# Performance work log

Measured on AMD Instinct MI355X. Metric: run time of the kernel, lower is better.

Reference implementation:

```python
import jax, jax.numpy as jnp
import numpy as np

NQ = 4
PI_HALF = np.pi / 2
HAD = jnp.array([[1, 1], [1, -1]], dtype=jnp.complex64) / np.sqrt(2)
CNOT = jnp.array([[1, 0, 0, 0], [0, 1, 0, 0], [0, 0, 0, 1], [0, 0, 1, 0]], dtype=jnp.complex64)
_bits = (np.arange(2 ** NQ)[:, None] >> np.arange(NQ - 1, -1, -1)[None, :]) & 1
ZSIGNS = jnp.asarray(1.0 - 2.0 * _bits, jnp.float32)  # [16, NQ]


def _ry(theta):
    c = jnp.cos(theta / 2).astype(jnp.complex64)
    s = jnp.sin(theta / 2).astype(jnp.complex64)
    return jnp.stack([jnp.stack([c, -s], -1), jnp.stack([s, c], -1)], -2)  # [...,2,2]


def _rot(phi, theta, omega):
    # PennyLane Rot = RZ(omega) @ RY(theta) @ RZ(phi)
    c = jnp.cos(theta / 2).astype(jnp.complex64)
    s = jnp.sin(theta / 2).astype(jnp.complex64)
    ep = jnp.exp(0.5j * phi).astype(jnp.complex64)
    eo = jnp.exp(0.5j * omega).astype(jnp.complex64)
    return jnp.stack([jnp.stack([jnp.conj(ep) * jnp.conj(eo) * c, -ep * jnp.conj(eo) * s]),
                      jnp.stack([jnp.conj(ep) * eo * s, ep * eo * c])])


def _cry(theta):
    # controlled-RY, batched: [B] -> [B,4,4], basis order (control, target)
    B = theta.shape[0]
    U = jnp.zeros((B, 4, 4), jnp.complex64).at[:, 0, 0].set(1.0).at[:, 1, 1].set(1.0)
    return U.at[:, 2:, 2:].set(_ry(theta))


def _apply1(state, U, wire):
    s = jnp.moveaxis(state, wire + 1, 1)
    shp = s.shape
    s = s.reshape(shp[0], 2, -1)
    s = jnp.einsum('ij,bjk->bik', U, s) if U.ndim == 2 else jnp.einsum('bij,bjk->bik', U, s)
    return jnp.moveaxis(s.reshape(shp), 1, wire + 1)


def _apply2(state, U, q0, q1):
    s = jnp.moveaxis(state, (q0 + 1, q1 + 1), (1, 2))
    shp = s.shape
    s = s.reshape(shp[0], 4, -1)
    s = jnp.einsum('ij,bjk->bik', U, s) if U.ndim == 2 else jnp.einsum('bij,bjk->bik', U, s)
    return jnp.moveaxis(s.reshape(shp), (1, 2), (q0 + 1, q1 + 1))


def _init_state(B):
    s = jnp.zeros((B, 2 ** NQ), jnp.complex64).at[:, 0].set(1.0)
    return s.reshape((B,) + (2,) * NQ)


def _zexp(state):
    p = state.reshape(state.shape[0], -1)
    p = p.real ** 2 + p.imag ** 2
    return p @ ZSIGNS  # [B, NQ]


def _attention_circuit(q, k, params):
    # q, k: [E, NQ] angles; params: [NQ, 3] shared
    s = _init_state(q.shape[0])
    for i in range(NQ):
        s = _apply1(s, _ry(q[:, i]), i)
    for i in range(NQ):
        s = _apply1(s, HAD, i)
    for i in range(NQ):
        s = _apply2(s, _cry(k[:, i]), i, (i + 1) % NQ)
    for i in range(NQ):
        s = _apply1(s, _rot(params[i, 0], params[i, 1], params[i, 2]), i)
    return _zexp(s)


def _entangle_circuit(x, params):
    # x: [N, NQ] angles; params: [n_layers, NQ, 3]
    s = _init_state(x.shape[0])
    for i in range(NQ):
        s = _apply1(s, _ry(x[:, i]), i)
    for l in range(params.shape[0]):
        for i in range(NQ - 1):
            s = _apply2(s, CNOT, i, i + 1)
        for i in range(NQ):
            s = _apply1(s, _rot(params[l, i, 0], params[l, i, 1], params[l, i, 2]), i)
        s = _apply2(s, CNOT, 0, NQ - 1)  # n_qubits >= 4
    return _zexp(s)


def _path_circuit(x, params):
    # x: [N, NQ]; params: [3, NQ, 3]
    s = _init_state(x.shape[0])
    for i in range(NQ):
        s = _apply1(s, HAD, i)
    for i in range(NQ):
        s = _apply1(s, _ry(x[:, i]), i)
    for l in range(3):
        for i in range(NQ):
            s = _apply1(s, _rot(params[l, i, 0], params[l, i, 1], params[l, i, 2]), i)
        for i in range(NQ - 1):
            s = _apply2(s, CNOT, i, i + 1)
    return _zexp(s)


def _forward(x, W_in, b_in, lin_W, lin_b, qproj_W, qproj_b, ent_params,
             attq_W, attq_b, attk_W, attk_b, att_qp, path_params,
             path_in_W, path_in_b, path_out_W, path_out_b, out_W, out_b, edge_index):
    N = x.shape[0]
    loops = jnp.arange(N, dtype=edge_index.dtype)
    ei = jnp.concatenate([edge_index, jnp.stack([loops, loops])], axis=1)  # add_self_loops
    src, dst = ei[0], ei[1]
    h = jax.nn.relu(x @ W_in.T + b_in)
    for l in range(lin_W.shape[0]):
        x_cls = h @ lin_W[l].T + lin_b[l]
        xq = _entangle_circuit(jnp.tanh(h[:, :NQ]) * PI_HALF, ent_params[l])
        x_comb = x_cls + xq @ qproj_W[l].T + qproj_b[l]
        q = jnp.tanh(h @ attq_W[l].T + attq_b[l]) * PI_HALF
        k = jnp.tanh(h @ attk_W[l].T + attk_b[l]) * PI_HALF
        scores = _attention_circuit(q[src], k[dst], att_qp[l]).mean(axis=1)  # [E]
        att = jax.nn.softmax(scores)  # global softmax over all edges (faithful)
        h = jax.ops.segment_sum(att[:, None] * x_comb[src], dst, num_segments=N)
        h = jax.nn.relu(h)  # dropout is identity at eval
    pq = jnp.tanh(h @ path_in_W.T + path_in_b) * PI_HALF
    h = _path_circuit(pq, path_params) @ path_out_W.T + path_out_b
    return h @ out_W.T + out_b


def setup_inputs() -> dict:
    key = jax.random.key(0)
    ks = jax.random.split(key, 22)
    N, E, D_in, D_h, D_out, L = 20000, 300000, 64, 128, 32, 2
    w = lambda k, shape: jax.random.normal(k, shape, jnp.float32) * 0.1
    return {
        'x': jax.random.normal(ks[0], (N, D_in), jnp.float32),
        'W_in': w(ks[1], (D_h, D_in)), 'b_in': w(ks[2], (D_h,)),
        'lin_W': w(ks[3], (L, D_h, D_h)), 'lin_b': w(ks[4], (L, D_h)),
        'qproj_W': w(ks[5], (L, D_h, NQ)), 'qproj_b': w(ks[6], (L, D_h)),
        'ent_params': w(ks[7], (L, 2, NQ, 3)),
        'attq_W': w(ks[8], (L, NQ, D_h)), 'attq_b': w(ks[9], (L, NQ)),
        'attk_W': w(ks[10], (L, NQ, D_h)), 'attk_b': w(ks[11], (L, NQ)),
        'att_qp': w(ks[12], (L, NQ, 3)),
        'path_params': w(ks[13], (3, NQ, 3)),
        'path_in_W': w(ks[14], (NQ, D_h)), 'path_in_b': w(ks[15], (NQ,)),
        'path_out_W': w(ks[16], (D_h, NQ)), 'path_out_b': w(ks[17], (D_h,)),
        'out_W': w(ks[18], (D_out, D_h)), 'out_b': w(ks[19], (D_out,)),
        'edge_index': jax.random.randint(ks[20], (2, E), 0, N, dtype=jnp.int32),
    }


def reference(x, W_in, b_in, lin_W, lin_b, qproj_W, qproj_b, ent_params,
              attq_W, attq_b, attk_W, attk_b, att_qp, path_params,
              path_in_W, path_in_b, path_out_W, path_out_b, out_W, out_b, edge_index):
    return _forward(x, W_in, b_in, lin_W, lin_b, qproj_W, qproj_b, ent_params,
                    attq_W, attq_b, attk_W, attk_b, att_qp, path_params,
                    path_in_W, path_in_b, path_out_W, path_out_b, out_W, out_b, edge_index)
```

## Files before the change

kernel.cpp:

```cpp
#include <hip/hip_runtime.h>
#include <math.h>

#define PI_HALF 1.57079632679489662f

__device__ __forceinline__ float fast_tanh(float x) {
    float e = __expf(2.f * x);
    return 1.f - 2.f * __builtin_amdgcn_rcpf(e + 1.f);
}


__device__ __forceinline__ void prod_init(float sr[16],
        float c0, float s0, float c1, float s1,
        float c2, float s2, float c3, float s3) {
    float p2[4];
    p2[0] = c0 * c1; p2[1] = c0 * s1; p2[2] = s0 * c1; p2[3] = s0 * s1;
    float p3[8];
#pragma unroll
    for (int j = 0; j < 4; ++j) { p3[2 * j] = p2[j] * c2; p3[2 * j + 1] = p2[j] * s2; }
#pragma unroll
    for (int j = 0; j < 8; ++j) { sr[2 * j] = p3[j] * c3; sr[2 * j + 1] = p3[j] * s3; }
}

template<int M>
__device__ __forceinline__ void had_r(float sr[16]) {
    const float r = 0.70710678118654752f;
#pragma unroll
    for (int i = 0; i < 16; ++i) {
        if (i & M) continue;
        const int j = i | M;
        float ar = sr[i], br = sr[j];
        sr[i] = (ar + br) * r;
        sr[j] = (ar - br) * r;
    }
}

template<int MC, int MT>
__device__ __forceinline__ void cry_r(float sr[16], float c, float s) {
#pragma unroll
    for (int i = 0; i < 16; ++i) {
        if (!(i & MC) || (i & MT)) continue;
        const int j = i | MT;
        float ar = sr[i], br = sr[j];
        sr[i] = c * ar - s * br;
        sr[j] = s * ar + c * br;
    }
}

template<int MC, int MT>
__device__ __forceinline__ void cnot_r(float sr[16]) {
#pragma unroll
    for (int i = 0; i < 16; ++i) {
        if (!(i & MC) || (i & MT)) continue;
        const int j = i | MT;
        float t = sr[i]; sr[i] = sr[j]; sr[j] = t;
    }
}

template<int MC, int MT>
__device__ __forceinline__ void cnot_g(float sr[16], float si[16]) {
#pragma unroll
    for (int i = 0; i < 16; ++i) {
        if (!(i & MC) || (i & MT)) continue;
        const int j = i | MT;
        float tr = sr[i], ti = si[i];
        sr[i] = sr[j]; si[i] = si[j];
        sr[j] = tr;    si[j] = ti;
    }
}

template<int M>
__device__ __forceinline__ void rot_pre(float sr[16], float si[16], const float* __restrict__ u) {
    const float u00r = u[0], u00i = u[1], u01r = u[2], u01i = u[3];
    const float u10r = u[4], u10i = u[5], u11r = u[6], u11i = u[7];
#pragma unroll
    for (int i = 0; i < 16; ++i) {
        if (i & M) continue;
        const int j = i | M;
        float ar = sr[i], ai = si[i], br = sr[j], bi = si[j];
        sr[i] = u00r * ar - u00i * ai + u01r * br - u01i * bi;
        si[i] = u00r * ai + u00i * ar + u01r * bi + u01i * br;
        sr[j] = u10r * ar - u10i * ai + u11r * br - u11i * bi;
        si[j] = u10r * ai + u10i * ar + u11r * bi + u11i * br;
    }
}

template<int M>
__device__ __forceinline__ void rot_first(float sr[16], float si[16], const float* __restrict__ u) {
    const float u00r = u[0], u00i = u[1], u01r = u[2], u01i = u[3];
    const float u10r = u[4], u10i = u[5], u11r = u[6], u11i = u[7];
#pragma unroll
    for (int i = 0; i < 16; ++i) {
        if (i & M) continue;
        const int j = i | M;
        float ar = sr[i], br = sr[j];
        sr[i] = u00r * ar + u01r * br;
        si[i] = u00i * ar + u01i * br;
        sr[j] = u10r * ar + u11r * br;
        si[j] = u10i * ar + u11i * br;
    }
}

__device__ __forceinline__ void zexp_g(const float sr[16], const float si[16], float z[4]) {
    float p[16];
#pragma unroll
    for (int i = 0; i < 16; ++i) p[i] = sr[i] * sr[i] + si[i] * si[i];
    z[0] = z[1] = z[2] = z[3] = 0.f;
#pragma unroll
    for (int i = 0; i < 16; ++i) {
        z[0] += (i & 8) ? -p[i] : p[i];
        z[1] += (i & 4) ? -p[i] : p[i];
        z[2] += (i & 2) ? -p[i] : p[i];
        z[3] += (i & 1) ? -p[i] : p[i];
    }
}


__global__ void k_fsi(const int* __restrict__ ei, int* __restrict__ cur,
                      int* __restrict__ srcs, int* __restrict__ inv, int E, int EP,
                      const float* __restrict__ entp, const float* __restrict__ attqp,
                      const float* __restrict__ pparm,
                      const float* __restrict__ outW, const float* __restrict__ outb,
                      const float* __restrict__ poW, const float* __restrict__ pob,
                      float* __restrict__ rotbuf, float* __restrict__ M,
                      float* __restrict__ v,
                      const float* __restrict__ x, const float* __restrict__ W,
                      const float* __restrict__ b, float* __restrict__ h,
                      int N, int eblocks) {
    __shared__ float xs[32 * 64];
    const int bb = blockIdx.x;
    const int tid = threadIdx.x;
    if (bb < eblocks) {
        int e = bb * 256 + tid;
        if (e < EP) {
            int s_, d_;
            if (e < E) { s_ = ei[e]; d_ = ei[E + e]; } else { s_ = d_ = e - E; }
            int pos = atomicAdd(&cur[d_], 1);
            srcs[pos] = s_;
            inv[e] = pos;
        }
        return;
    }
    if (bb == eblocks) {
        const int t = tid;
        if (t < 36) {
            const float* p;
            if (t < 16)      p = entp  + t * 3;
            else if (t < 24) p = attqp + (t - 16) * 3;
            else             p = pparm + (t - 24) * 3;
            float phi = p[0], theta = p[1], omega = p[2];
            float st, ct; sincosf(0.5f * theta, &st, &ct);
            float sp, cp; sincosf(0.5f * (phi + omega), &sp, &cp);
            float sm, cm; sincosf(0.5f * (phi - omega), &sm, &cm);
            float* u = rotbuf + t * 8;
            u[0] =  ct * cp;  u[1] = -ct * sp;
            u[2] = -st * cm;  u[3] = -st * sm;
            u[4] =  st * cm;  u[5] = -st * sm;
            u[6] =  ct * cp;  u[7] =  ct * sp;
        } else if (t >= 64 && t < 192) {
            int t2 = t - 64;
            int o = t2 >> 2, i = t2 & 3;
            float acc = 0.f;
            for (int j = 0; j < 128; ++j) acc += outW[o * 128 + j] * poW[j * 4 + i];
            M[t2] = acc;
        } else if (t >= 192 && t < 224) {
            int o = t - 192;
            float acc = outb[o];
            for (int j = 0; j < 128; ++j) acc += outW[o * 128 + j] * pob[j];
            v[o] = acc;
        }
        return;
    }
    const int base = (bb - eblocks - 1) * 32;
    for (int idx = tid; idx < 32 * 64; idx += 256) {
        int n = base + (idx >> 6);
        xs[idx] = (n < N) ? x[(size_t)n * 64 + (idx & 63)] : 0.f;
    }
    __syncthreads();
    const int ch = tid & 127;
    const int half = tid >> 7;
    float acc[16];
#pragma unroll
    for (int n = 0; n < 16; ++n) acc[n] = 0.f;
    const float4* wr4 = (const float4*)(W + ch * 64);
    for (int c4 = 0; c4 < 16; ++c4) {
        float4 w = wr4[c4];
#pragma unroll
        for (int n = 0; n < 16; ++n) {
            float4 hv = *(const float4*)&xs[(half * 16 + n) * 64 + c4 * 4];
            acc[n] += w.x * hv.x + w.y * hv.y + w.z * hv.z + w.w * hv.w;
        }
    }
    const float bbv = b[ch];
#pragma unroll
    for (int n = 0; n < 16; ++n) {
        int node = base + half * 16 + n;
        if (node < N) h[(size_t)node * 128 + ch] = fmaxf(acc[n] + bbv, 0.f);
    }
}

__global__ void k_entlin(const float* __restrict__ h, const float* __restrict__ rotE2,
                         const float* __restrict__ linW, const float* __restrict__ linb,
                         const float* __restrict__ qpW, const float* __restrict__ qpb,
                         const float* __restrict__ aqW, const float* __restrict__ aqb,
                         const float* __restrict__ akW, const float* __restrict__ akb,
                         float* __restrict__ xcomb, float* __restrict__ qbuf,
                         float* __restrict__ kbuf, int N) {
    __shared__ float hs[16 * 128];
    __shared__ float xqs[16 * 4];
    const int base = blockIdx.x * 16;
    const int tid = threadIdx.x;
    for (int idx = tid; idx < 16 * 128; idx += 128) {
        int n = base + (idx >> 7);
        hs[idx] = (n < N) ? h[(size_t)n * 128 + (idx & 127)] : 0.f;
    }
    __syncthreads();
    if (tid < 16) {
        float4 hv = *(const float4*)&hs[tid * 128];
        float c0, s0, c1, s1, c2, s2, c3, s3;
        { float a = fast_tanh(hv.x) * (0.5f * PI_HALF); __sincosf(a, &s0, &c0); }
        { float a = fast_tanh(hv.y) * (0.5f * PI_HALF); __sincosf(a, &s1, &c1); }
        { float a = fast_tanh(hv.z) * (0.5f * PI_HALF); __sincosf(a, &s2, &c2); }
        { float a = fast_tanh(hv.w) * (0.5f * PI_HALF); __sincosf(a, &s3, &c3); }
        float sr[16], si[16];
        prod_init(sr, c0, s0, c1, s1, c2, s2, c3, s3);
        cnot_r<8, 4>(sr); cnot_r<4, 2>(sr); cnot_r<2, 1>(sr);
        rot_first<8>(sr, si, rotE2);
        rot_pre<4>(sr, si, rotE2 + 8);
        rot_pre<2>(sr, si, rotE2 + 16);
        rot_pre<1>(sr, si, rotE2 + 24);
        cnot_g<8, 1>(sr, si);
        cnot_g<8, 4>(sr, si); cnot_g<4, 2>(sr, si); cnot_g<2, 1>(sr, si);
        const float* P = rotE2 + 32;
        rot_pre<8>(sr, si, P);
        rot_pre<4>(sr, si, P + 8);
        rot_pre<2>(sr, si, P + 16);
        rot_pre<1>(sr, si, P + 24);
        cnot_g<8, 1>(sr, si);
        float z[4]; zexp_g(sr, si, z);
        xqs[tid * 4 + 0] = z[0]; xqs[tid * 4 + 1] = z[1];
        xqs[tid * 4 + 2] = z[2]; xqs[tid * 4 + 3] = z[3];
    }
    __syncthreads();
    float acc[16];
#pragma unroll
    for (int n = 0; n < 16; ++n) acc[n] = 0.f;
    const float4* wr4 = (const float4*)(linW + tid * 128);
    for (int c4 = 0; c4 < 32; ++c4) {
        float4 w = wr4[c4];
#pragma unroll
        for (int n = 0; n < 16; ++n) {
            float4 hv = *(const float4*)&hs[n * 128 + c4 * 4];
            acc[n] += w.x * hv.x + w.y * hv.y + w.z * hv.z + w.w * hv.w;
        }
    }
    const float bb = linb[tid] + qpb[tid];
    const float qw0 = qpW[tid * 4 + 0], qw1 = qpW[tid * 4 + 1];
    const float qw2 = qpW[tid * 4 + 2], qw3 = qpW[tid * 4 + 3];
#pragma unroll
    for (int n = 0; n < 16; ++n) {
        int node = base + n;
        if (node < N) {
            xcomb[(size_t)node * 128 + tid] = acc[n] + bb
                + qw0 * xqs[n * 4 + 0] + qw1 * xqs[n * 4 + 1]
                + qw2 * xqs[n * 4 + 2] + qw3 * xqs[n * 4 + 3];
        }
    }
    const int nl = tid >> 3;
    const int which = tid & 7;
    const int qi = which & 3;
    const float4* Wp4 = (const float4*)(((which < 4) ? aqW : akW) + qi * 128);
    float dot = (which < 4) ? aqb[qi] : akb[qi];
    for (int c4 = 0; c4 < 32; ++c4) {
        float4 w = Wp4[c4];
        float4 hv = *(const float4*)&hs[nl * 128 + c4 * 4];
        dot += w.x * hv.x + w.y * hv.y + w.z * hv.z + w.w * hv.w;
    }
    int node = base + nl;
    if (node < N) {
        float halfang = fast_tanh(dot) * (0.5f * PI_HALF);
        float s, c; __sincosf(halfang, &s, &c);
        float* dst = ((which < 4) ? qbuf : kbuf) + (size_t)node * 8 + qi * 2;
        dst[0] = c; dst[1] = s;
    }
}

__global__ void k_att(const float* __restrict__ qb, const float* __restrict__ kb,
                      const int* __restrict__ ei, const float* __restrict__ RA,
                      const int* __restrict__ inv, float* __restrict__ escore,
                      float* __restrict__ sumexp, int E, int EP) {
    __shared__ float red[4];
    int e = blockIdx.x * blockDim.x + threadIdx.x;
    float ex = 0.f;
    if (e < EP) {
        int s_, d_;
        if (e < E) { s_ = ei[e]; d_ = ei[E + e]; } else { s_ = d_ = e - E; }
        float4 qa = *(const float4*)&qb[(size_t)s_ * 8];
        float4 qc = *(const float4*)&qb[(size_t)s_ * 8 + 4];
        float4 ka = *(const float4*)&kb[(size_t)d_ * 8];
        float4 kc = *(const float4*)&kb[(size_t)d_ * 8 + 4];
        float sr[16], si[16];
        prod_init(sr, qa.x, qa.y, qa.z, qa.w, qc.x, qc.y, qc.z, qc.w);
        had_r<8>(sr); had_r<4>(sr); had_r<2>(sr); had_r<1>(sr);
        cry_r<8, 4>(sr, ka.x, ka.y);
        cry_r<4, 2>(sr, ka.z, ka.w);
        cry_r<2, 1>(sr, kc.x, kc.y);
        cry_r<1, 8>(sr, kc.z, kc.w);
        rot_first<8>(sr, si, RA);
        rot_pre<4>(sr, si, RA + 8);
        rot_pre<2>(sr, si, RA + 16);
        rot_pre<1>(sr, si, RA + 24);
        float p0  = sr[0]  * sr[0]  + si[0]  * si[0];
        float p1  = sr[1]  * sr[1]  + si[1]  * si[1];
        float p2  = sr[2]  * sr[2]  + si[2]  * si[2];
        float p4  = sr[4]  * sr[4]  + si[4]  * si[4];
        float p8  = sr[8]  * sr[8]  + si[8]  * si[8];
        float p7  = sr[7]  * sr[7]  + si[7]  * si[7];
        float p11 = sr[11] * sr[11] + si[11] * si[11];
        float p13 = sr[13] * sr[13] + si[13] * si[13];
        float p14 = sr[14] * sr[14] + si[14] * si[14];
        float p15 = sr[15] * sr[15] + si[15] * si[15];
        float sc = (p0 - p15) + 0.5f * ((p1 + p2 + p4 + p8) - (p7 + p11 + p13 + p14));
        ex = __expf(sc);
        escore[inv[e]] = ex;
    }
    float wsum = ex;
#pragma unroll
    for (int d = 32; d; d >>= 1) wsum += __shfl_xor(wsum, d, 64);
    if ((threadIdx.x & 63) == 0) red[threadIdx.x >> 6] = wsum;
    __syncthreads();
    if (threadIdx.x == 0) atomicAdd(sumexp, red[0] + red[1] + red[2] + red[3]);
}


__global__ void k_hist(const int* __restrict__ ei, int* __restrict__ cnt, int E, int EP) {
    int e = blockIdx.x * blockDim.x + threadIdx.x;
    if (e >= EP) return;
    int d_ = (e < E) ? ei[E + e] : e - E;
    atomicAdd(&cnt[d_], 1);
}

__global__ void k_scan(const int* __restrict__ cnt, int* __restrict__ off,
                       int* __restrict__ cur, int N) {
    __shared__ int tot[1024];
    const int t = threadIdx.x;
    const int chunk = (N + 1023) >> 10;
    const int s0 = t * chunk;
    const int s1 = min(s0 + chunk, N);
    int sum = 0;
    for (int i = s0; i < s1; ++i) sum += cnt[i];
    tot[t] = sum;
    __syncthreads();
    for (int d = 1; d < 1024; d <<= 1) {
        int v = (t >= d) ? tot[t - d] : 0;
        __syncthreads();
        tot[t] += v;
        __syncthreads();
    }
    int run = (t == 0) ? 0 : tot[t - 1];
    for (int i = s0; i < s1; ++i) {
        off[i] = run; cur[i] = run;
        run += cnt[i];
    }
}

__global__ void k_gather(const float* __restrict__ xcomb, const int* __restrict__ srcs,
                         const float* __restrict__ escore, const int* __restrict__ off,
                         const int* __restrict__ cnt, const float* __restrict__ sumexp,
                         float* __restrict__ h) {
    __shared__ int sS[128];
    __shared__ float wS[128];
    const int b = blockIdx.x;
    const int tid = threadIdx.x;
    const int start = off[b];
    const int num = cnt[b];
    float acc = 0.f;
    for (int base = 0; base < num; base += 128) {
        int m = min(128, num - base);
        if (tid < m) {
            sS[tid] = srcs[start + base + tid];
            wS[tid] = escore[start + base + tid];
        }
        __syncthreads();
        for (int i = 0; i < m; ++i)
            acc += wS[i] * xcomb[(size_t)sS[i] * 128 + tid];
        __syncthreads();
    }
    const float invS = __builtin_amdgcn_rcpf(sumexp[0]);
    h[(size_t)b * 128 + tid] = fmaxf(acc * invS, 0.f);
}

__global__ void k_tail(const float* __restrict__ h, const float* __restrict__ piW,
                       const float* __restrict__ pib, const float* __restrict__ RP,
                       const float* __restrict__ M, const float* __restrict__ v,
                       float* __restrict__ out, int N) {
    __shared__ float pqS[64 * 8];
    __shared__ float zS[64 * 4];
    __shared__ float MS[128];
    __shared__ float vS[32];
    const int tid = threadIdx.x;
    const int base = blockIdx.x * 64;
    if (tid < 128) MS[tid] = M[tid];
    else if (tid < 160) vS[tid - 128] = v[tid - 128];
    {
        const int nl = tid >> 2, i = tid & 3;
        const int node = base + nl;
        if (node < N) {
            float dot = pib[i];
            const float4* w4 = (const float4*)(piW + i * 128);
            const float4* h4 = (const float4*)(h + (size_t)node * 128);
#pragma unroll 8
            for (int c4 = 0; c4 < 32; ++c4) {
                float4 w = w4[c4];
                float4 hv = h4[c4];
                dot += w.x * hv.x + w.y * hv.y + w.z * hv.z + w.w * hv.w;
            }
            float halfang = fast_tanh(dot) * (0.5f * PI_HALF);
            float s, c; __sincosf(halfang, &s, &c);
            pqS[nl * 8 + i * 2]     = c;
            pqS[nl * 8 + i * 2 + 1] = s;
        }
    }
    __syncthreads();
    if (tid < 64 && base + tid < N) {
        const float r = 0.70710678118654752f;
        float c0 = pqS[tid * 8 + 0], s0 = pqS[tid * 8 + 1];
        float c1 = pqS[tid * 8 + 2], s1 = pqS[tid * 8 + 3];
        float c2 = pqS[tid * 8 + 4], s2 = pqS[tid * 8 + 5];
        float c3 = pqS[tid * 8 + 6], s3 = pqS[tid * 8 + 7];
        float u0 = r * (c0 - s0), w0 = r * (c0 + s0);
        float u1 = r * (c1 - s1), w1 = r * (c1 + s1);
        float u2 = r * (c2 - s2), w2 = r * (c2 + s2);
        float u3 = r * (c3 - s3), w3 = r * (c3 + s3);
        float sr[16], si[16];
        prod_init(sr, u0, w0, u1, w1, u2, w2, u3, w3);
        rot_first<8>(sr, si, RP);
        rot_pre<4>(sr, si, RP + 8);
        rot_pre<2>(sr, si, RP + 16);
        rot_pre<1>(sr, si, RP + 24);
        cnot_g<8, 4>(sr, si); cnot_g<4, 2>(sr, si); cnot_g<2, 1>(sr, si);
#pragma unroll
        for (int l = 1; l < 3; ++l) {
            const float* P = RP + l * 32;
            rot_pre<8>(sr, si, P);
            rot_pre<4>(sr, si, P + 8);
            rot_pre<2>(sr, si, P + 16);
            rot_pre<1>(sr, si, P + 24);
            cnot_g<8, 4>(sr, si); cnot_g<4, 2>(sr, si); cnot_g<2, 1>(sr, si);
        }
        float z[4]; zexp_g(sr, si, z);
        zS[tid * 4 + 0] = z[0]; zS[tid * 4 + 1] = z[1];
        zS[tid * 4 + 2] = z[2]; zS[tid * 4 + 3] = z[3];
    }
    __syncthreads();
#pragma unroll
    for (int k = 0; k < 8; ++k) {
        int flat = k * 256 + tid;
        int nl = flat >> 5;
        int o = flat & 31;
        int node = base + nl;
        if (node < N) {
            out[(size_t)node * 32 + o] = vS[o]
                + MS[o * 4 + 0] * zS[nl * 4 + 0] + MS[o * 4 + 1] * zS[nl * 4 + 1]
                + MS[o * 4 + 2] * zS[nl * 4 + 2] + MS[o * 4 + 3] * zS[nl * 4 + 3];
        }
    }
}


extern "C" void kernel_launch(void* const* d_in, const int* in_sizes, int n_in,
                              void* d_out, int out_size, void* d_ws, size_t ws_size,
                              hipStream_t stream) {
    const float* x     = (const float*)d_in[0];
    const float* W_in  = (const float*)d_in[1];
    const float* b_in  = (const float*)d_in[2];
    const float* linW  = (const float*)d_in[3];
    const float* linb  = (const float*)d_in[4];
    const float* qpW   = (const float*)d_in[5];
    const float* qpb   = (const float*)d_in[6];
    const float* entp  = (const float*)d_in[7];
    const float* aqW   = (const float*)d_in[8];
    const float* aqb   = (const float*)d_in[9];
    const float* akW   = (const float*)d_in[10];
    const float* akb   = (const float*)d_in[11];
    const float* attqp = (const float*)d_in[12];
    const float* pparm = (const float*)d_in[13];
    const float* piW   = (const float*)d_in[14];
    const float* pib   = (const float*)d_in[15];
    const float* poW   = (const float*)d_in[16];
    const float* pob   = (const float*)d_in[17];
    const float* outW  = (const float*)d_in[18];
    const float* outb  = (const float*)d_in[19];
    const int*   ei    = (const int*)d_in[20];

    const int N  = in_sizes[0] / 64;
    const int E  = in_sizes[20] / 2;
    const int EP = E + N;

    float* ws     = (float*)d_ws;
    float* h      = ws;
    float* xcomb  = h      + (size_t)N * 128;
    float* qbuf   = xcomb  + (size_t)N * 128;
    float* kbuf   = qbuf   + (size_t)N * 8;
    float* escore = kbuf   + (size_t)N * 8;
    float* rotbuf = escore + EP;
    float* Mm     = rotbuf + 36 * 8;
    float* vv     = Mm + 128;
    int*   cnt    = (int*)(vv + 32);
    float* sumexp = (float*)(cnt + N);
    int*   off    = (int*)(sumexp + 4);
    int*   cur    = off + N;
    int*   srcs   = cur + N;
    int*   inv    = srcs + EP;

    const float* rotE = rotbuf;
    const float* rotA = rotbuf + 128;
    const float* rotP = rotbuf + 192;

    const int nb16 = (N + 15) / 16;
    const int nb32 = (N + 31) / 32;
    const int ebl  = (EP + 255) / 256;

    hipMemsetAsync(cnt, 0, (size_t)(N + 4) * sizeof(int), stream);
    k_hist<<<ebl, 256, 0, stream>>>(ei, cnt, E, EP);
    k_scan<<<1, 1024, 0, stream>>>(cnt, off, cur, N);
    k_fsi<<<ebl + 1 + nb32, 256, 0, stream>>>(ei, cur, srcs, inv, E, EP,
                                              entp, attqp, pparm, outW, outb, poW, pob,
                                              rotbuf, Mm, vv, x, W_in, b_in, h, N, ebl);

    for (int l = 0; l < 2; ++l) {
        k_entlin<<<nb16, 128, 0, stream>>>(h, rotE + l * 64,
            linW + (size_t)l * 128 * 128, linb + l * 128,
            qpW + (size_t)l * 128 * 4, qpb + l * 128,
            aqW + (size_t)l * 4 * 128, aqb + l * 4,
            akW + (size_t)l * 4 * 128, akb + l * 4,
            xcomb, qbuf, kbuf, N);
        k_att<<<ebl, 256, 0, stream>>>(qbuf, kbuf, ei, rotA + l * 32, inv,
                                       escore, sumexp + l, E, EP);
        k_gather<<<N, 128, 0, stream>>>(xcomb, srcs, escore, off, cnt, sumexp + l, h);
    }

    k_tail<<<(N + 63) / 64, 256, 0, stream>>>(h, piW, pib, rotP, Mm, vv, (float*)d_out, N);
}
```

Measured before the change: 381.4 us.

## Restructure entangle-linear kernel: overlap circuit with projections, 2-channel register tiling

Reworks k_entlin so the attention q/k projections run on one wavefront while the per-node quantum circuit runs on a second wavefront concurrently, instead of serialising the circuit before the other work. The linear layer now gives each thread two output channels over 8 nodes, so every shared-memory h value is reused for two weights. The h tile is loaded with float4 accesses into a padded stride-132 layout. This cuts one block barrier phase and the idle threads during the circuit, at the cost of more registers per thread and less parallel work across channels.

```diff
diff --git a/kernel.cpp b/kernel.cpp
--- a/kernel.cpp
+++ b/kernel.cpp
@@ -198,6 +198,7 @@
     }
 }
 
+#define HS_STRIDE 132
 __global__ void k_entlin(const float* __restrict__ h, const float* __restrict__ rotE2,
                          const float* __restrict__ linW, const float* __restrict__ linb,
                          const float* __restrict__ qpW, const float* __restrict__ qpb,
@@ -205,82 +206,106 @@
                          const float* __restrict__ akW, const float* __restrict__ akb,
                          float* __restrict__ xcomb, float* __restrict__ qbuf,
                          float* __restrict__ kbuf, int N) {
-    __shared__ float hs[16 * 128];
+    __shared__ float hs[16 * HS_STRIDE];
     __shared__ float xqs[16 * 4];
     const int base = blockIdx.x * 16;
     const int tid = threadIdx.x;
-    for (int idx = tid; idx < 16 * 128; idx += 128) {
-        int n = base + (idx >> 7);
-        hs[idx] = (n < N) ? h[(size_t)n * 128 + (idx & 127)] : 0.f;
-    }
-    __syncthreads();
-    if (tid < 16) {
-        float4 hv = *(const float4*)&hs[tid * 128];
-        float c0, s0, c1, s1, c2, s2, c3, s3;
-        { float a = fast_tanh(hv.x) * (0.5f * PI_HALF); __sincosf(a, &s0, &c0); }
-        { float a = fast_tanh(hv.y) * (0.5f * PI_HALF); __sincosf(a, &s1, &c1); }
-        { float a = fast_tanh(hv.z) * (0.5f * PI_HALF); __sincosf(a, &s2, &c2); }
-        { float a = fast_tanh(hv.w) * (0.5f * PI_HALF); __sincosf(a, &s3, &c3); }
-        float sr[16], si[16];
-        prod_init(sr, c0, s0, c1, s1, c2, s2, c3, s3);
-        cnot_r<8, 4>(sr); cnot_r<4, 2>(sr); cnot_r<2, 1>(sr);
-        rot_first<8>(sr, si, rotE2);
-        rot_pre<4>(sr, si, rotE2 + 8);
-        rot_pre<2>(sr, si, rotE2 + 16);
-        rot_pre<1>(sr, si, rotE2 + 24);
-        cnot_g<8, 1>(sr, si);
-        cnot_g<8, 4>(sr, si); cnot_g<4, 2>(sr, si); cnot_g<2, 1>(sr, si);
-        const float* P = rotE2 + 32;
-        rot_pre<8>(sr, si, P);
-        rot_pre<4>(sr, si, P + 8);
-        rot_pre<2>(sr, si, P + 16);
-        rot_pre<1>(sr, si, P + 24);
-        cnot_g<8, 1>(sr, si);
-        float z[4]; zexp_g(sr, si, z);
-        xqs[tid * 4 + 0] = z[0]; xqs[tid * 4 + 1] = z[1];
-        xqs[tid * 4 + 2] = z[2]; xqs[tid * 4 + 3] = z[3];
-    }
-    __syncthreads();
-    float acc[16];
-#pragma unroll
-    for (int n = 0; n < 16; ++n) acc[n] = 0.f;
-    const float4* wr4 = (const float4*)(linW + tid * 128);
+    for (int idx = tid; idx < 16 * 32; idx += 128) {
+        int n = idx >> 5, c4 = idx & 31;
+        int node = base + n;
+        float4 hv = (node < N) ? *(const float4*)&h[(size_t)node * 128 + c4 * 4]
+                               : make_float4(0.f, 0.f, 0.f, 0.f);
+        *(float4*)&hs[n * HS_STRIDE + c4 * 4] = hv;
+    }
+    __syncthreads();
+    if (tid < 64) {
+#pragma unroll
+        for (int rep = 0; rep < 2; ++rep) {
+            const int dt = tid + rep * 64;
+            const int nl = dt >> 3;
+            const int which = dt & 7;
+            const int qi = which & 3;
+            const float4* Wp4 = (const float4*)(((which < 4) ? aqW : akW) + qi * 128);
+            float dot = (which < 4) ? aqb[qi] : akb[qi];
+            for (int c4 = 0; c4 < 32; ++c4) {
+                float4 w = Wp4[c4];
+                float4 hv = *(const float4*)&hs[nl * HS_STRIDE + c4 * 4];
+                dot += w.x * hv.x + w.y * hv.y + w.z * hv.z + w.w * hv.w;
+            }
+            int node = base + nl;
+            if (node < N) {
+                float halfang = fast_tanh(dot) * (0.5f * PI_HALF);
+                float s, c; __sincosf(halfang, &s, &c);
+                float* dst = ((which < 4) ? qbuf : kbuf) + (size_t)node * 8 + qi * 2;
+                dst[0] = c; dst[1] = s;
+            }
+        }
+    } else if (tid < 80) {
+        const int nl = tid - 64;
+        if (base + nl < N) {
+            float4 hv = *(const float4*)&hs[nl * HS_STRIDE];
+            float c0, s0, c1, s1, c2, s2, c3, s3;
+            { float a = fast_tanh(hv.x) * (0.5f * PI_HALF); __sincosf(a, &s0, &c0); }
+            { float a = fast_tanh(hv.y) * (0.5f * PI_HALF); __sincosf(a, &s1, &c1); }
+            { float a = fast_tanh(hv.z) * (0.5f * PI_HALF); __sincosf(a, &s2, &c2); }
+            { float a = fast_tanh(hv.w) * (0.5f * PI_HALF); __sincosf(a, &s3, &c3); }
+            float sr[16], si[16];
+            prod_init(sr, c0, s0, c1, s1, c2, s2, c3, s3);
+            cnot_r<8, 4>(sr); cnot_r<4, 2>(sr); cnot_r<2, 1>(sr);
+            rot_first<8>(sr, si, rotE2);
+            rot_pre<4>(sr, si, rotE2 + 8);
+            rot_pre<2>(sr, si, rotE2 + 16);
+            rot_pre<1>(sr, si, rotE2 + 24);
+            cnot_g<8, 1>(sr, si);
+            cnot_g<8, 4>(sr, si); cnot_g<4, 2>(sr, si); cnot_g<2, 1>(sr, si);
+            const float* P = rotE2 + 32;
+            rot_pre<8>(sr, si, P);
+            rot_pre<4>(sr, si, P + 8);
+            rot_pre<2>(sr, si, P + 16);
+            rot_pre<1>(sr, si, P + 24);
+            cnot_g<8, 1>(sr, si);
+            float z[4]; zexp_g(sr, si, z);
+            xqs[nl * 4 + 0] = z[0]; xqs[nl * 4 + 1] = z[1];
+            xqs[nl * 4 + 2] = z[2]; xqs[nl * 4 + 3] = z[3];
+        }
+    }
+    __syncthreads();
+    const int lane = tid & 63;
+    const int nh = tid >> 6;
+    const int ch0 = lane, ch1 = lane + 64;
+    float acc0[8], acc1[8];
+#pragma unroll
+    for (int n = 0; n < 8; ++n) { acc0[n] = 0.f; acc1[n] = 0.f; }
+    const float4* w04 = (const float4*)(linW + ch0 * 128);
+    const float4* w14 = (const float4*)(linW + ch1 * 128);
     for (int c4 = 0; c4 < 32; ++c4) {
-        float4 w = wr4[c4];
-#pragma unroll
-        for (int n = 0; n < 16; ++n) {
-            float4 hv = *(const float4*)&hs[n * 128 + c4 * 4];
-            acc[n] += w.x * hv.x + w.y * hv.y + w.z * hv.z + w.w * hv.w;
-        }
-    }
-    const float bb = linb[tid] + qpb[tid];
-    const float qw0 = qpW[tid * 4 + 0], qw1 = qpW[tid * 4 + 1];
-    const float qw2 = qpW[tid * 4 + 2], qw3 = qpW[tid * 4 + 3];
-#pragma unroll
-    for (int n = 0; n < 16; ++n) {
-        int node = base + n;
+        float4 wa = w04[c4];
+        float4 wb = w14[c4];
+#pragma unroll
+        for (int n = 0; n < 8; ++n) {
+            float4 hv = *(const float4*)&hs[(nh * 8 + n) * HS_STRIDE + c4 * 4];
+            acc0[n] += wa.x * hv.x + wa.y * hv.y + wa.z * hv.z + wa.w * hv.w;
+            acc1[n] += wb.x * hv.x + wb.y * hv.y + wb.z * hv.z + wb.w * hv.w;
+        }
+    }
+    const float b0 = linb[ch0] + qpb[ch0];
+    const float b1 = linb[ch1] + qpb[ch1];
+    const float q00 = qpW[ch0 * 4 + 0], q01 = qpW[ch0 * 4 + 1];
+    const float q02 = qpW[ch0 * 4 + 2], q03 = qpW[ch0 * 4 + 3];
+    const float q10 = qpW[ch1 * 4 + 0], q11 = qpW[ch1 * 4 + 1];
+    const float q12 = qpW[ch1 * 4 + 2], q13 = qpW[ch1 * 4 + 3];
+#pragma unroll
+    for (int n = 0; n < 8; ++n) {
+        const int nl = nh * 8 + n;
+        const int node = base + nl;
         if (node < N) {
-            xcomb[(size_t)node * 128 + tid] = acc[n] + bb
-                + qw0 * xqs[n * 4 + 0] + qw1 * xqs[n * 4 + 1]
-                + qw2 * xqs[n * 4 + 2] + qw3 * xqs[n * 4 + 3];
-        }
-    }
-    const int nl = tid >> 3;
-    const int which = tid & 7;
-    const int qi = which & 3;
-    const float4* Wp4 = (const float4*)(((which < 4) ? aqW : akW) + qi * 128);
-    float dot = (which < 4) ? aqb[qi] : akb[qi];
-    for (int c4 = 0; c4 < 32; ++c4) {
-        float4 w = Wp4[c4];
-        float4 hv = *(const float4*)&hs[nl * 128 + c4 * 4];
-        dot += w.x * hv.x + w.y * hv.y + w.z * hv.z + w.w * hv.w;
-    }
-    int node = base + nl;
-    if (node < N) {
-        float halfang = fast_tanh(dot) * (0.5f * PI_HALF);
-        float s, c; __sincosf(halfang, &s, &c);
-        float* dst = ((which < 4) ? qbuf : kbuf) + (size_t)node * 8 + qi * 2;
-        dst[0] = c; dst[1] = s;
+            float x0 = xqs[nl * 4 + 0], x1 = xqs[nl * 4 + 1];
+            float x2 = xqs[nl * 4 + 2], x3 = xqs[nl * 4 + 3];
+            xcomb[(size_t)node * 128 + ch0] = acc0[n] + b0
+                + q00 * x0 + q01 * x1 + q02 * x2 + q03 * x3;
+            xcomb[(size_t)node * 128 + ch1] = acc1[n] + b1
+                + q10 * x0 + q11 * x1 + q12 * x2 + q13 * x3;
+        }
     }
 }
 
```

After: 355.5 us. 1.07x faster.
